# Optimization experiments

Measured on AMD Instinct MI355X. Metric: run time of the kernel, lower is better.

The kernel has to match this reference:

```python
import jax, jax.numpy as jnp
import numpy as np


def setup_inputs() -> dict:
    key = jax.random.key(0)
    ks = jax.random.split(key, 5)
    B, C, H, W = 8, 256, 64, 64
    Ck = C // 8  # 32, reduced channel dim
    return {
        "x": jax.random.normal(ks[0], (B, C, H, W), dtype=jnp.float32),
        "wf": jax.random.normal(ks[1], (Ck, C), dtype=jnp.float32) * 0.05,
        "wg": jax.random.normal(ks[2], (Ck, C), dtype=jnp.float32) * 0.05,
        "wh": jax.random.normal(ks[3], (Ck, C), dtype=jnp.float32) * 0.05,
        "wv": jax.random.normal(ks[4], (C, Ck), dtype=jnp.float32) * 0.05,
        "gamma": jnp.zeros((1,), dtype=jnp.float32),
    }


def reference(x, wf, wg, wh, wv, gamma):
    B, C, H, W = x.shape
    N = H * W
    xf = x.reshape(B, C, N)  # flatten spatial tokens
    # 1x1 convs == channel matmuls
    f = jnp.einsum('oc,bcn->bon', wf, xf)  # [B, Ck, N]
    g = jnp.einsum('oc,bcn->bon', wg, xf)  # [B, Ck, N]
    h = jnp.einsum('oc,bcn->bon', wh, xf)  # [B, Ck, N]
    # s = f^T @ g -> [B, N, N]; softmax over last axis (dim 2 in torch)
    s = jnp.einsum('bcn,bcm->bnm', f, g)
    beta = jax.nn.softmax(s, axis=2)
    # v = h @ beta  (note: beta NOT transposed, faithful to original)
    v = jnp.einsum('bcn,bnm->bcm', h, beta)  # [B, Ck, N]
    o = jnp.einsum('oc,bcm->bom', wv, v).reshape(B, C, H, W)
    return gamma * o + x
```

## Files before the change

kernel.cpp:

```cpp
#include <hip/hip_runtime.h>
#include <hip/hip_bf16.h>

#define BB 8
#define CC 256
#define CK 32
#define NN 4096

typedef short bf16x8 __attribute__((ext_vector_type(8)));
typedef float f32x4 __attribute__((ext_vector_type(4)));

#define MFMA(a, b, c) __builtin_amdgcn_mfma_f32_16x16x32_bf16((a), (b), (c), 0, 0, 0)

#define GLOAD16(gsrc, ldst) __builtin_amdgcn_global_load_lds( \
    (const __attribute__((address_space(1))) void*)(gsrc), \
    (__attribute__((address_space(3))) void*)(ldst), 16, 0, 0)

#define OBASE(b) ((size_t)(b) * 1048576)
#define OFF_F  0
#define OFF_G  65536
#define OFF_HT 131072
#define OFF_LE 196608
#define OFF_V0 200704
#define OFF_XB 524288
#define OFF_WB 786432
#define VSTRIDE 131072

#define SHIFT 24.0f

static __device__ __forceinline__ unsigned pack_trunc(float lo, float hi) {
  unsigned ulo = __builtin_bit_cast(unsigned, lo);
  unsigned uhi = __builtin_bit_cast(unsigned, hi);
  return (uhi & 0xFFFF0000u) | (ulo >> 16);
}
static __device__ __forceinline__ unsigned pack_rne(float lo, float hi) {
  unsigned ulo = __builtin_bit_cast(unsigned, lo);
  unsigned uhi = __builtin_bit_cast(unsigned, hi);
  ulo += 0x7FFFu + ((ulo >> 16) & 1u);
  uhi += 0x7FFFu + ((uhi >> 16) & 1u);
  return (uhi & 0xFFFF0000u) | (ulo >> 16);
}
static __device__ __forceinline__ unsigned short rne16(float v) {
  unsigned u = __builtin_bit_cast(unsigned, v);
  u += 0x7FFFu + ((u >> 16) & 1u);
  return (unsigned short)(u >> 16);
}

__global__ __launch_bounds__(256) void cvt_kernel(
    const float* __restrict__ x, const float* __restrict__ wf,
    const float* __restrict__ wg, const float* __restrict__ wh,
    float* __restrict__ sc)
{
  int blk = blockIdx.x;
  int tid = threadIdx.x;
  if (blk >= 2048) {
    unsigned short* wb = (unsigned short*)(sc + OFF_WB);
    const float* srcs[3] = {wf, wg, wh};
    #pragma unroll 1
    for (int w = 0; w < 3; ++w) {
      const float* src = srcs[w];
      for (int e = tid; e < 8192; e += 256) wb[w * 8192 + e] = rne16(src[e]);
    }
    return;
  }
  __shared__ float t[64][69];
  int b = blk >> 8, r = blk & 255, nt = r >> 2, ct = r & 3;
  int n0 = nt << 6, c0 = ct << 6;
  const float* xb = x + ((size_t)b * CC + c0) * NN + n0;
  int ci0 = tid >> 4, j = (tid & 15) << 2;
  #pragma unroll
  for (int p = 0; p < 4; ++p) {
    int ci = p * 16 + ci0;
    float4 v = *(const float4*)&xb[(size_t)ci * NN + j];
    t[ci][j] = v.x; t[ci][j + 1] = v.y; t[ci][j + 2] = v.z; t[ci][j + 3] = v.w;
  }
  __syncthreads();
  int ni = tid >> 2, cq = (tid & 3) << 4;
  unsigned u[8];
  #pragma unroll
  for (int e = 0; e < 8; ++e)
    u[e] = pack_rne(t[cq + 2 * e][ni], t[cq + 2 * e + 1][ni]);
  unsigned short* xbf = (unsigned short*)(sc + OBASE(b) + OFF_XB);
  unsigned* dst = (unsigned*)(xbf + (size_t)(n0 + ni) * CC + c0 + cq);
  *(uint4*)dst       = make_uint4(u[0], u[1], u[2], u[3]);
  *(uint4*)(dst + 4) = make_uint4(u[4], u[5], u[6], u[7]);
}

__global__ __launch_bounds__(256) void projmm_kernel(float* __restrict__ sc)
{
  int tid = threadIdx.x, blk = blockIdx.x;
  int b = blk >> 6, nblk = blk & 63;
  int w = tid >> 6, lane = tid & 63, q = lane >> 4, c = lane & 15;
  int nb = (nblk << 6) + (w << 4);

  const char* xB = (const char*)(sc + OBASE(b) + OFF_XB);
  const char* wB = (const char*)(sc + OFF_WB);

  const f32x4 z4 = {0.f, 0.f, 0.f, 0.f};
  f32x4 fa0 = z4, fa1 = z4, ga0 = z4, ga1 = z4, ha0 = z4, ha1 = z4;

  #pragma unroll
  for (int kc = 0; kc < 8; ++kc) {
    int ko = kc * 64 + q * 16;
    bf16x8 xa = *(const bf16x8*)(xB + (size_t)(nb + c) * 512 + ko);
    bf16x8 w0 = *(const bf16x8*)(wB + (size_t)c * 512 + ko);
    bf16x8 w1 = *(const bf16x8*)(wB + (size_t)(16 + c) * 512 + ko);
    bf16x8 w2 = *(const bf16x8*)(wB + 16384 + (size_t)c * 512 + ko);
    bf16x8 w3 = *(const bf16x8*)(wB + 16384 + (size_t)(16 + c) * 512 + ko);
    bf16x8 w4 = *(const bf16x8*)(wB + 32768 + (size_t)c * 512 + ko);
    bf16x8 w5 = *(const bf16x8*)(wB + 32768 + (size_t)(16 + c) * 512 + ko);
    fa0 = MFMA(xa, w0, fa0);  fa1 = MFMA(xa, w1, fa1);
    ga0 = MFMA(xa, w2, ga0);  ga1 = MFMA(xa, w3, ga1);
    ha0 = MFMA(w4, xa, ha0);  ha1 = MFMA(w5, xa, ha1);
  }

  unsigned short* fD = (unsigned short*)(sc + OBASE(b) + OFF_F);
  unsigned short* gD = (unsigned short*)(sc + OBASE(b) + OFF_G);
  unsigned short* hD = (unsigned short*)(sc + OBASE(b) + OFF_HT);
  #pragma unroll
  for (int r = 0; r < 4; ++r) {
    int n = nb + q * 4 + r;
    fD[(size_t)n * 32 + c]      = rne16(fa0[r]);
    fD[(size_t)n * 32 + 16 + c] = rne16(fa1[r]);
    gD[(size_t)n * 32 + c]      = rne16(ga0[r]);
    gD[(size_t)n * 32 + 16 + c] = rne16(ga1[r]);
    hD[(size_t)(q * 4 + r) * NN + nb + c]        = rne16(ha0[r]);
    hD[(size_t)(16 + q * 4 + r) * NN + nb + c]   = rne16(ha1[r]);
  }
}

__global__ __launch_bounds__(256) void passb_kernel(float* __restrict__ sc)
{
  __shared__ float Zsh[2][16][4];
  int tid = threadIdx.x, blk = blockIdx.x;
  int b = blk >> 7, nb0 = (blk & 127) << 5;
  int w = tid >> 6, lane = tid & 63, q = lane >> 4, c = lane & 15;

  const char* fb = (const char*)(sc + OBASE(b) + OFF_F);
  const char* gb = (const char*)(sc + OBASE(b) + OFF_G);

  bf16x8 fa0 = *(const bf16x8*)(fb + (size_t)(nb0 + c) * 64 + q * 16);
  bf16x8 fa1 = *(const bf16x8*)(fb + (size_t)(nb0 + 16 + c) * 64 + q * 16);
  const f32x4 z4 = {0.f, 0.f, 0.f, 0.f};
  float za[2][4] = {{0.f,0.f,0.f,0.f},{0.f,0.f,0.f,0.f}};

  int mt0 = w << 10;
  bf16x8 g0 = *(const bf16x8*)(gb + (size_t)(mt0 + 0  + c) * 64 + q * 16);
  bf16x8 g1 = *(const bf16x8*)(gb + (size_t)(mt0 + 16 + c) * 64 + q * 16);
  bf16x8 g2 = *(const bf16x8*)(gb + (size_t)(mt0 + 32 + c) * 64 + q * 16);
  bf16x8 g3 = *(const bf16x8*)(gb + (size_t)(mt0 + 48 + c) * 64 + q * 16);

  for (int mt = mt0; mt < mt0 + 1024; mt += 64) {
    int mtn = (mt + 64 < mt0 + 1024) ? mt + 64 : mt0;
    bf16x8 n0 = *(const bf16x8*)(gb + (size_t)(mtn + 0  + c) * 64 + q * 16);
    bf16x8 n1 = *(const bf16x8*)(gb + (size_t)(mtn + 16 + c) * 64 + q * 16);
    bf16x8 n2 = *(const bf16x8*)(gb + (size_t)(mtn + 32 + c) * 64 + q * 16);
    bf16x8 n3 = *(const bf16x8*)(gb + (size_t)(mtn + 48 + c) * 64 + q * 16);
    f32x4 s;
    #define BSTEP(gk) \
      s = MFMA(fa0, gk, z4); \
      za[0][0] += __expf(s[0] - SHIFT); za[0][1] += __expf(s[1] - SHIFT); \
      za[0][2] += __expf(s[2] - SHIFT); za[0][3] += __expf(s[3] - SHIFT); \
      s = MFMA(fa1, gk, z4); \
      za[1][0] += __expf(s[0] - SHIFT); za[1][1] += __expf(s[1] - SHIFT); \
      za[1][2] += __expf(s[2] - SHIFT); za[1][3] += __expf(s[3] - SHIFT);
    BSTEP(g0) BSTEP(g1) BSTEP(g2) BSTEP(g3)
    #undef BSTEP
    g0 = n0; g1 = n1; g2 = n2; g3 = n3;
  }
  #pragma unroll
  for (int d = 1; d < 16; d <<= 1) {
    #pragma unroll
    for (int i = 0; i < 2; ++i)
      #pragma unroll
      for (int r = 0; r < 4; ++r) za[i][r] += __shfl_xor(za[i][r], d);
  }
  if (c == 0) {
    #pragma unroll
    for (int i = 0; i < 2; ++i)
      #pragma unroll
      for (int r = 0; r < 4; ++r) Zsh[i][q * 4 + r][w] = za[i][r];
  }
  __syncthreads();
  if (tid < 32) {
    int ns2 = tid >> 4, row = tid & 15;
    float Z = Zsh[ns2][row][0] + Zsh[ns2][row][1]
            + Zsh[ns2][row][2] + Zsh[ns2][row][3];
    sc[OBASE(b) + OFF_LE + nb0 + ns2 * 16 + row] = SHIFT + __logf(Z);
  }
}

__global__ __launch_bounds__(256, 4) void passc_kernel(float* __restrict__ sc)
{
  __shared__ unsigned Pt[128 * 32];
  __shared__ float Lsh[1024];
  __shared__ unsigned fsh[2][1024];
  __shared__ unsigned hsh[2][1024];

  int tid = threadIdx.x, blk = blockIdx.x;
  int b = blk >> 7, rest = blk & 127;
  int ns = rest & 3, mblk = rest >> 2;
  int m0 = mblk << 7;
  int nbase = ns << 10;
  int w = tid >> 6, lane = tid & 63, q = lane >> 4, c = lane & 15;
  int hc = tid >> 3, hslot = (tid & 7) ^ (hc & 7);

  const char* fb = (const char*)(sc + OBASE(b) + OFF_F);
  const char* gb = (const char*)(sc + OBASE(b) + OFF_G);
  const char* hb = (const char*)(sc + OBASE(b) + OFF_HT);
  const float* LE = sc + OBASE(b) + OFF_LE;

  for (int i = tid; i < 1024; i += 256) Lsh[i] = LE[nbase + i];

  bf16x8 gB0 = *(const bf16x8*)(gb + (size_t)(m0 + w * 16 + c) * 64 + q * 16);
  bf16x8 gB1 = *(const bf16x8*)(gb + (size_t)(m0 + 64 + w * 16 + c) * 64 + q * 16);

  GLOAD16(fb + (size_t)nbase * 64 + tid * 16, (char*)&fsh[0][0] + tid * 16);
  GLOAD16(hb + (size_t)hc * 8192 + (size_t)nbase * 2 + hslot * 16,
          (char*)&hsh[0][0] + tid * 16);
  __syncthreads();

  const f32x4 z4 = {0.f, 0.f, 0.f, 0.f};
  f32x4 v00 = z4, v01 = z4, v10 = z4, v11 = z4;

  unsigned sw = (unsigned)(c & 7) << 4;
  char* Pt0 = (char*)Pt + (size_t)(w * 16 + c) * 128;
  char* Pt1 = (char*)Pt + (size_t)(64 + w * 16 + c) * 128;

  int buf = 0;
  for (int nt = 0; nt < 1024; nt += 64) {
    if (nt + 64 < 1024) {
      GLOAD16(fb + (size_t)(nbase + nt + 64) * 64 + tid * 16,
              (char*)&fsh[buf ^ 1][0] + tid * 16);
      GLOAD16(hb + (size_t)hc * 8192 + (size_t)(nbase + nt + 64) * 2 + hslot * 16,
              (char*)&hsh[buf ^ 1][0] + tid * 16);
    }
    const char* fS = (const char*)&fsh[buf][0];
    const char* hS = (const char*)&hsh[buf][0];

    bf16x8 f0 = *(const bf16x8*)(fS + (0 * 16 + c) * 64 + q * 16);
    bf16x8 f1 = *(const bf16x8*)(fS + (1 * 16 + c) * 64 + q * 16);
    bf16x8 f2 = *(const bf16x8*)(fS + (2 * 16 + c) * 64 + q * 16);
    bf16x8 f3 = *(const bf16x8*)(fS + (3 * 16 + c) * 64 + q * 16);
    f32x4 sA0 = MFMA(f0, gB0, z4), sB0 = MFMA(f0, gB1, z4);
    f32x4 sA1 = MFMA(f1, gB0, z4), sB1 = MFMA(f1, gB1, z4);
    f32x4 sA2 = MFMA(f2, gB0, z4), sB2 = MFMA(f2, gB1, z4);
    f32x4 sA3 = MFMA(f3, gB0, z4), sB3 = MFMA(f3, gB1, z4);

    #pragma unroll
    for (int sub = 0; sub < 4; ++sub) {
      f32x4 sA = (sub == 0) ? sA0 : (sub == 1) ? sA1 : (sub == 2) ? sA2 : sA3;
      f32x4 sB = (sub == 0) ? sB0 : (sub == 1) ? sB1 : (sub == 2) ? sB2 : sB3;
      const f32x4 Lt = *(const f32x4*)&Lsh[nt + sub * 16 + q * 4];
      uint2 pkA, pkB;
      pkA.x = pack_trunc(__expf(sA[0] - Lt[0]), __expf(sA[1] - Lt[1]));
      pkA.y = pack_trunc(__expf(sA[2] - Lt[2]), __expf(sA[3] - Lt[3]));
      pkB.x = pack_trunc(__expf(sB[0] - Lt[0]), __expf(sB[1] - Lt[1]));
      pkB.y = pack_trunc(__expf(sB[2] - Lt[2]), __expf(sB[3] - Lt[3]));
      unsigned off = ((unsigned)(sub * 32 + q * 8)) ^ sw;
      *(uint2*)(Pt0 + off) = pkA;
      *(uint2*)(Pt1 + off) = pkB;
    }

    #pragma unroll
    for (int ks = 0; ks < 2; ++ks) {
      unsigned off = ((unsigned)(ks * 64 + q * 16)) ^ sw;
      bf16x8 pb0 = *(const bf16x8*)(Pt0 + off);
      bf16x8 pb1 = *(const bf16x8*)(Pt1 + off);
      unsigned hoff = ((unsigned)(ks * 64 + q * 16)) ^ sw;
      bf16x8 h0 = *(const bf16x8*)(hS + c * 128 + hoff);
      bf16x8 h1 = *(const bf16x8*)(hS + (16 + c) * 128 + hoff);
      v00 = MFMA(h0, pb0, v00);
      v10 = MFMA(h1, pb0, v10);
      v01 = MFMA(h0, pb1, v01);
      v11 = MFMA(h1, pb1, v11);
    }
    __syncthreads();
    buf ^= 1;
  }

  float* V = sc + OBASE(b) + OFF_V0 + (size_t)ns * VSTRIDE;
  {
    int mA = m0 + w * 16 + c, mB = m0 + 64 + w * 16 + c;
    size_t bA = (size_t)(mA & 31) * 4096 + (size_t)(mA >> 5) * 32;
    size_t bB = (size_t)(mB & 31) * 4096 + (size_t)(mB >> 5) * 32;
    *(f32x4*)&V[bA + q * 4]      = v00;
    *(f32x4*)&V[bA + 16 + q * 4] = v10;
    *(f32x4*)&V[bB + q * 4]      = v01;
    *(f32x4*)&V[bB + 16 + q * 4] = v11;
  }
}

__global__ __launch_bounds__(256) void epi_kernel(
    float* out, const float* __restrict__ x,
    const float* __restrict__ wv, const float* __restrict__ gamma)
{
  int tid = threadIdx.x, blk = blockIdx.x;
  int b = blk >> 7;
  int m0 = (blk & 127) << 5;
  int w = tid >> 6, lane = tid & 63, q = lane >> 4, c = lane & 15;
  int co0 = w << 6;

  const float* V0 = out + OBASE(b) + OFF_V0;

  bf16x8 Bf[2];
  #pragma unroll
  for (int mt = 0; mt < 2; ++mt) {
    int ml = mt * 16 + c;
    size_t base = (size_t)ml * 4096 + (size_t)(m0 >> 5) * 32 + q * 8;
    float4 a0 = {0,0,0,0}, a1 = {0,0,0,0};
    #pragma unroll
    for (int i = 0; i < 4; ++i) {
      const float* Vi = V0 + (size_t)i * VSTRIDE;
      float4 p0 = *(const float4*)&Vi[base];
      float4 p1 = *(const float4*)&Vi[base + 4];
      a0.x += p0.x; a0.y += p0.y; a0.z += p0.z; a0.w += p0.w;
      a1.x += p1.x; a1.y += p1.y; a1.z += p1.z; a1.w += p1.w;
    }
    unsigned u0 = pack_rne(a0.x, a0.y);
    unsigned u1 = pack_rne(a0.z, a0.w);
    unsigned u2 = pack_rne(a1.x, a1.y);
    unsigned u3 = pack_rne(a1.z, a1.w);
    Bf[mt] = __builtin_bit_cast(bf16x8, make_uint4(u0, u1, u2, u3));
  }
  bf16x8 Af[4];
  #pragma unroll
  for (int ci = 0; ci < 4; ++ci) {
    const float* wr = wv + (size_t)(co0 + ci * 16 + c) * 32 + q * 8;
    float4 a0 = *(const float4*)wr;
    float4 a1 = *(const float4*)(wr + 4);
    unsigned u0 = pack_rne(a0.x, a0.y);
    unsigned u1 = pack_rne(a0.z, a0.w);
    unsigned u2 = pack_rne(a1.x, a1.y);
    unsigned u3 = pack_rne(a1.z, a1.w);
    Af[ci] = __builtin_bit_cast(bf16x8, make_uint4(u0, u1, u2, u3));
  }
  __syncthreads();

  const f32x4 z4 = {0.f, 0.f, 0.f, 0.f};
  const float g0 = gamma[0];
  #pragma unroll
  for (int ci = 0; ci < 4; ++ci) {
    #pragma unroll
    for (int mt = 0; mt < 2; ++mt) {
      f32x4 acc = MFMA(Af[ci], Bf[mt], z4);
      #pragma unroll
      for (int r = 0; r < 4; ++r) {
        int co = co0 + ci * 16 + q * 4 + r;
        size_t idx = ((size_t)b * CC + co) * NN + m0 + mt * 16 + c;
        out[idx] = g0 * acc[r] + x[idx];
      }
    }
  }
}

extern "C" void kernel_launch(void* const* d_in, const int* in_sizes, int n_in,
                              void* d_out, int out_size, void* d_ws, size_t ws_size,
                              hipStream_t stream) {
  const float* x     = (const float*)d_in[0];
  const float* wf    = (const float*)d_in[1];
  const float* wg    = (const float*)d_in[2];
  const float* wh    = (const float*)d_in[3];
  const float* wv    = (const float*)d_in[4];
  const float* gamma = (const float*)d_in[5];
  float* out = (float*)d_out;

  cvt_kernel   <<<2049, 256, 0, stream>>>(x, wf, wg, wh, out);
  projmm_kernel<<<512,  256, 0, stream>>>(out);
  passb_kernel <<<1024, 256, 0, stream>>>(out);
  passc_kernel <<<1024, 256, 0, stream>>>(out);
  epi_kernel   <<<1024, 256, 0, stream>>>(out, x, wv, gamma);
}
```

Before: 120.6 us.

## Fold softmax normalizer into h, use exp2 and hardware bf16 pack in passc

Pass B now computes 1/Z per query row and scales the transposed h values in place by it, so pass C no longer loads per-row log-normalizers or subtracts them before exponentiation. Exponentials switch to exp2 with a fused multiply-add against a constant shift, and packing to bf16 uses the hardware v_cvt_pk_bf16_f32 instruction. The f tile in LDS gets an XOR swizzle to cut bank conflicts, and passc's occupancy hint rises from 4 to 5. The trade-off is an extra rounding of h to bf16 after normalization, plus a fixed shift that must keep exp2 inside range.

Result: slower. 143.4 us (+19.0%).

```diff
diff --git a/kernel.cpp b/kernel.cpp
--- a/kernel.cpp
+++ b/kernel.cpp
@@ -19,19 +19,14 @@
 #define OFF_F  0
 #define OFF_G  65536
 #define OFF_HT 131072
-#define OFF_LE 196608
 #define OFF_V0 200704
 #define OFF_XB 524288
 #define OFF_WB 786432
 #define VSTRIDE 131072
 
-#define SHIFT 24.0f
-
-static __device__ __forceinline__ unsigned pack_trunc(float lo, float hi) {
-  unsigned ulo = __builtin_bit_cast(unsigned, lo);
-  unsigned uhi = __builtin_bit_cast(unsigned, hi);
-  return (uhi & 0xFFFF0000u) | (ulo >> 16);
-}
+#define L2E 1.44269504089f
+#define S2  34.6246810188f
+
 static __device__ __forceinline__ unsigned pack_rne(float lo, float hi) {
   unsigned ulo = __builtin_bit_cast(unsigned, lo);
   unsigned uhi = __builtin_bit_cast(unsigned, hi);
@@ -43,6 +38,14 @@
   unsigned u = __builtin_bit_cast(unsigned, v);
   u += 0x7FFFu + ((u >> 16) & 1u);
   return (unsigned short)(u >> 16);
+}
+static __device__ __forceinline__ unsigned pk_bf162(float lo, float hi) {
+  unsigned r;
+  asm("v_cvt_pk_bf16_f32 %0, %1, %2" : "=v"(r) : "v"(lo), "v"(hi));
+  return r;
+}
+static __device__ __forceinline__ float fexp2(float y) {
+  return __builtin_exp2f(y);
 }
 
 __global__ __launch_bounds__(256) void cvt_kernel(
@@ -131,6 +134,7 @@
 __global__ __launch_bounds__(256) void passb_kernel(float* __restrict__ sc)
 {
   __shared__ float Zsh[2][16][4];
+  __shared__ float Rsh[32];
   int tid = threadIdx.x, blk = blockIdx.x;
   int b = blk >> 7, nb0 = (blk & 127) << 5;
   int w = tid >> 6, lane = tid & 63, q = lane >> 4, c = lane & 15;
@@ -158,11 +162,11 @@
     f32x4 s;
     #define BSTEP(gk) \
       s = MFMA(fa0, gk, z4); \
-      za[0][0] += __expf(s[0] - SHIFT); za[0][1] += __expf(s[1] - SHIFT); \
-      za[0][2] += __expf(s[2] - SHIFT); za[0][3] += __expf(s[3] - SHIFT); \
+      za[0][0] += fexp2(fmaf(s[0], L2E, -S2)); za[0][1] += fexp2(fmaf(s[1], L2E, -S2)); \
+      za[0][2] += fexp2(fmaf(s[2], L2E, -S2)); za[0][3] += fexp2(fmaf(s[3], L2E, -S2)); \
       s = MFMA(fa1, gk, z4); \
-      za[1][0] += __expf(s[0] - SHIFT); za[1][1] += __expf(s[1] - SHIFT); \
-      za[1][2] += __expf(s[2] - SHIFT); za[1][3] += __expf(s[3] - SHIFT);
+      za[1][0] += fexp2(fmaf(s[0], L2E, -S2)); za[1][1] += fexp2(fmaf(s[1], L2E, -S2)); \
+      za[1][2] += fexp2(fmaf(s[2], L2E, -S2)); za[1][3] += fexp2(fmaf(s[3], L2E, -S2));
     BSTEP(g0) BSTEP(g1) BSTEP(g2) BSTEP(g3)
     #undef BSTEP
     g0 = n0; g1 = n1; g2 = n2; g3 = n3;
@@ -185,14 +189,28 @@
     int ns2 = tid >> 4, row = tid & 15;
     float Z = Zsh[ns2][row][0] + Zsh[ns2][row][1]
             + Zsh[ns2][row][2] + Zsh[ns2][row][3];
-    sc[OBASE(b) + OFF_LE + nb0 + ns2 * 16 + row] = SHIFT + __logf(Z);
-  }
-}
-
-__global__ __launch_bounds__(256, 4) void passc_kernel(float* __restrict__ sc)
+    Rsh[ns2 * 16 + row] = 1.0f / Z;
+  }
+  __syncthreads();
+  {
+    int cidx = tid >> 3, jj = (tid & 7) << 2;
+    unsigned short* hp = (unsigned short*)(sc + OBASE(b) + OFF_HT)
+                       + (size_t)cidx * NN + nb0 + jj;
+    uint2 hv = *(const uint2*)hp;
+    float h0 = __builtin_bit_cast(float, hv.x << 16)          * Rsh[jj + 0];
+    float h1 = __builtin_bit_cast(float, hv.x & 0xFFFF0000u)  * Rsh[jj + 1];
+    float h2 = __builtin_bit_cast(float, hv.y << 16)          * Rsh[jj + 2];
+    float h3 = __builtin_bit_cast(float, hv.y & 0xFFFF0000u)  * Rsh[jj + 3];
+    uint2 ov;
+    ov.x = pack_rne(h0, h1);
+    ov.y = pack_rne(h2, h3);
+    *(uint2*)hp = ov;
+  }
+}
+
+__global__ __launch_bounds__(256, 5) void passc_kernel(float* __restrict__ sc)
 {
   __shared__ unsigned Pt[128 * 32];
-  __shared__ float Lsh[1024];
   __shared__ unsigned fsh[2][1024];
   __shared__ unsigned hsh[2][1024];
 
@@ -203,18 +221,18 @@
   int nbase = ns << 10;
   int w = tid >> 6, lane = tid & 63, q = lane >> 4, c = lane & 15;
   int hc = tid >> 3, hslot = (tid & 7) ^ (hc & 7);
+  size_t fso = (size_t)(tid >> 2) * 64
+             + (size_t)(((tid & 3) ^ ((tid >> 3) & 3)) * 16);
+  int fsw = (c >> 1) & 3;
 
   const char* fb = (const char*)(sc + OBASE(b) + OFF_F);
   const char* gb = (const char*)(sc + OBASE(b) + OFF_G);
   const char* hb = (const char*)(sc + OBASE(b) + OFF_HT);
-  const float* LE = sc + OBASE(b) + OFF_LE;
-
-  for (int i = tid; i < 1024; i += 256) Lsh[i] = LE[nbase + i];
 
   bf16x8 gB0 = *(const bf16x8*)(gb + (size_t)(m0 + w * 16 + c) * 64 + q * 16);
   bf16x8 gB1 = *(const bf16x8*)(gb + (size_t)(m0 + 64 + w * 16 + c) * 64 + q * 16);
 
-  GLOAD16(fb + (size_t)nbase * 64 + tid * 16, (char*)&fsh[0][0] + tid * 16);
+  GLOAD16(fb + (size_t)nbase * 64 + fso, (char*)&fsh[0][0] + tid * 16);
   GLOAD16(hb + (size_t)hc * 8192 + (size_t)nbase * 2 + hslot * 16,
           (char*)&hsh[0][0] + tid * 16);
   __syncthreads();
@@ -229,7 +247,7 @@
   int buf = 0;
   for (int nt = 0; nt < 1024; nt += 64) {
     if (nt + 64 < 1024) {
-      GLOAD16(fb + (size_t)(nbase + nt + 64) * 64 + tid * 16,
+      GLOAD16(fb + (size_t)(nbase + nt + 64) * 64 + fso,
               (char*)&fsh[buf ^ 1][0] + tid * 16);
       GLOAD16(hb + (size_t)hc * 8192 + (size_t)(nbase + nt + 64) * 2 + hslot * 16,
               (char*)&hsh[buf ^ 1][0] + tid * 16);
@@ -237,10 +255,10 @@
     const char* fS = (const char*)&fsh[buf][0];
     const char* hS = (const char*)&hsh[buf][0];
 
-    bf16x8 f0 = *(const bf16x8*)(fS + (0 * 16 + c) * 64 + q * 16);
-    bf16x8 f1 = *(const bf16x8*)(fS + (1 * 16 + c) * 64 + q * 16);
-    bf16x8 f2 = *(const bf16x8*)(fS + (2 * 16 + c) * 64 + q * 16);
-    bf16x8 f3 = *(const bf16x8*)(fS + (3 * 16 + c) * 64 + q * 16);
+    bf16x8 f0 = *(const bf16x8*)(fS + (size_t)(0 * 16 + c) * 64 + ((q ^ fsw) * 16));
+    bf16x8 f1 = *(const bf16x8*)(fS + (size_t)(1 * 16 + c) * 64 + ((q ^ fsw) * 16));
+    bf16x8 f2 = *(const bf16x8*)(fS + (size_t)(2 * 16 + c) * 64 + ((q ^ fsw) * 16));
+    bf16x8 f3 = *(const bf16x8*)(fS + (size_t)(3 * 16 + c) * 64 + ((q ^ fsw) * 16));
     f32x4 sA0 = MFMA(f0, gB0, z4), sB0 = MFMA(f0, gB1, z4);
     f32x4 sA1 = MFMA(f1, gB0, z4), sB1 = MFMA(f1, gB1, z4);
     f32x4 sA2 = MFMA(f2, gB0, z4), sB2 = MFMA(f2, gB1, z4);
@@ -250,12 +268,11 @@
     for (int sub = 0; sub < 4; ++sub) {
       f32x4 sA = (sub == 0) ? sA0 : (sub == 1) ? sA1 : (sub == 2) ? sA2 : sA3;
       f32x4 sB = (sub == 0) ? sB0 : (sub == 1) ? sB1 : (sub == 2) ? sB2 : sB3;
-      const f32x4 Lt = *(const f32x4*)&Lsh[nt + sub * 16 + q * 4];
       uint2 pkA, pkB;
-      pkA.x = pack_trunc(__expf(sA[0] - Lt[0]), __expf(sA[1] - Lt[1]));
-      pkA.y = pack_trunc(__expf(sA[2] - Lt[2]), __expf(sA[3] - Lt[3]));
-      pkB.x = pack_trunc(__expf(sB[0] - Lt[0]), __expf(sB[1] - Lt[1]));
-      pkB.y = pack_trunc(__expf(sB[2] - Lt[2]), __expf(sB[3] - Lt[3]));
+      pkA.x = pk_bf162(fexp2(fmaf(sA[0], L2E, -S2)), fexp2(fmaf(sA[1], L2E, -S2)));
+      pkA.y = pk_bf162(fexp2(fmaf(sA[2], L2E, -S2)), fexp2(fmaf(sA[3], L2E, -S2)));
+      pkB.x = pk_bf162(fexp2(fmaf(sB[0], L2E, -S2)), fexp2(fmaf(sB[1], L2E, -S2)));
+      pkB.y = pk_bf162(fexp2(fmaf(sB[2], L2E, -S2)), fexp2(fmaf(sB[3], L2E, -S2)));
       unsigned off = ((unsigned)(sub * 32 + q * 8)) ^ sw;
       *(uint2*)(Pt0 + off) = pkA;
       *(uint2*)(Pt1 + off) = pkB;
@@ -266,9 +283,8 @@
       unsigned off = ((unsigned)(ks * 64 + q * 16)) ^ sw;
       bf16x8 pb0 = *(const bf16x8*)(Pt0 + off);
       bf16x8 pb1 = *(const bf16x8*)(Pt1 + off);
-      unsigned hoff = ((unsigned)(ks * 64 + q * 16)) ^ sw;
-      bf16x8 h0 = *(const bf16x8*)(hS + c * 128 + hoff);
-      bf16x8 h1 = *(const bf16x8*)(hS + (16 + c) * 128 + hoff);
+      bf16x8 h0 = *(const bf16x8*)(hS + c * 128 + off);
+      bf16x8 h1 = *(const bf16x8*)(hS + (16 + c) * 128 + off);
       v00 = MFMA(h0, pb0, v00);
       v10 = MFMA(h1, pb0, v10);
       v01 = MFMA(h0, pb1, v01);
```

## Fuse x-to-bf16 conversion into projection kernel via shared memory

Applied to the files above, without the earlier changes.

The x transpose and bf16 conversion now happen inside the projection kernel, which stages a 64-token by 256-channel bf16 tile in shared memory and feeds the MFMAs from it. This removes the global write and read of a bf16 copy of x, and weight conversion becomes a separate tiny 3-block kernel. In exchange each projection block loops over four channel tiles serially with two barriers each, and uses about 51KB of LDS, which lowers occupancy. A redundant offset computation in passc is also folded.

Result: faster. 108.8 us (-9.7%).

```diff
diff --git a/kernel.cpp b/kernel.cpp
--- a/kernel.cpp
+++ b/kernel.cpp
@@ -21,7 +21,6 @@
 #define OFF_HT 131072
 #define OFF_LE 196608
 #define OFF_V0 200704
-#define OFF_XB 524288
 #define OFF_WB 786432
 #define VSTRIDE 131072
 
@@ -45,63 +44,58 @@
   return (unsigned short)(u >> 16);
 }
 
-__global__ __launch_bounds__(256) void cvt_kernel(
-    const float* __restrict__ x, const float* __restrict__ wf,
-    const float* __restrict__ wg, const float* __restrict__ wh,
-    float* __restrict__ sc)
-{
-  int blk = blockIdx.x;
+__global__ __launch_bounds__(256) void wcvt_kernel(
+    const float* __restrict__ wf, const float* __restrict__ wg,
+    const float* __restrict__ wh, float* __restrict__ sc)
+{
+  int w = blockIdx.x;
   int tid = threadIdx.x;
-  if (blk >= 2048) {
-    unsigned short* wb = (unsigned short*)(sc + OFF_WB);
-    const float* srcs[3] = {wf, wg, wh};
-    #pragma unroll 1
-    for (int w = 0; w < 3; ++w) {
-      const float* src = srcs[w];
-      for (int e = tid; e < 8192; e += 256) wb[w * 8192 + e] = rne16(src[e]);
-    }
-    return;
-  }
+  const float* src = (w == 0) ? wf : ((w == 1) ? wg : wh);
+  unsigned short* wb = (unsigned short*)(sc + OFF_WB) + w * 8192;
+  for (int e = tid; e < 8192; e += 256) wb[e] = rne16(src[e]);
+}
+
+__global__ __launch_bounds__(256) void proj_kernel(
+    const float* __restrict__ x, float* __restrict__ sc)
+{
   __shared__ float t[64][69];
-  int b = blk >> 8, r = blk & 255, nt = r >> 2, ct = r & 3;
-  int n0 = nt << 6, c0 = ct << 6;
-  const float* xb = x + ((size_t)b * CC + c0) * NN + n0;
-  int ci0 = tid >> 4, j = (tid & 15) << 2;
-  #pragma unroll
-  for (int p = 0; p < 4; ++p) {
-    int ci = p * 16 + ci0;
-    float4 v = *(const float4*)&xb[(size_t)ci * NN + j];
-    t[ci][j] = v.x; t[ci][j + 1] = v.y; t[ci][j + 2] = v.z; t[ci][j + 3] = v.w;
-  }
-  __syncthreads();
-  int ni = tid >> 2, cq = (tid & 3) << 4;
-  unsigned u[8];
-  #pragma unroll
-  for (int e = 0; e < 8; ++e)
-    u[e] = pack_rne(t[cq + 2 * e][ni], t[cq + 2 * e + 1][ni]);
-  unsigned short* xbf = (unsigned short*)(sc + OBASE(b) + OFF_XB);
-  unsigned* dst = (unsigned*)(xbf + (size_t)(n0 + ni) * CC + c0 + cq);
-  *(uint4*)dst       = make_uint4(u[0], u[1], u[2], u[3]);
-  *(uint4*)(dst + 4) = make_uint4(u[4], u[5], u[6], u[7]);
-}
-
-__global__ __launch_bounds__(256) void projmm_kernel(float* __restrict__ sc)
-{
+  __shared__ unsigned short tb[64][264];
+
   int tid = threadIdx.x, blk = blockIdx.x;
-  int b = blk >> 6, nblk = blk & 63;
+  int b = blk >> 6, n0 = (blk & 63) << 6;
+
+  #pragma unroll 1
+  for (int ct = 0; ct < 4; ++ct) {
+    int c0 = ct << 6;
+    const float* xb = x + ((size_t)b * CC + c0) * NN + n0;
+    int ci0 = tid >> 4, j = (tid & 15) << 2;
+    #pragma unroll
+    for (int p = 0; p < 4; ++p) {
+      int ci = p * 16 + ci0;
+      float4 v = *(const float4*)&xb[(size_t)ci * NN + j];
+      t[ci][j] = v.x; t[ci][j + 1] = v.y; t[ci][j + 2] = v.z; t[ci][j + 3] = v.w;
+    }
+    __syncthreads();
+    int ni = tid >> 2, cq = (tid & 3) << 4;
+    #pragma unroll
+    for (int e = 0; e < 16; ++e)
+      tb[ni][c0 + cq + e] = rne16(t[cq + e][ni]);
+    __syncthreads();
+  }
+
   int w = tid >> 6, lane = tid & 63, q = lane >> 4, c = lane & 15;
-  int nb = (nblk << 6) + (w << 4);
-
-  const char* xB = (const char*)(sc + OBASE(b) + OFF_XB);
+  int nb = n0 + (w << 4);
   const char* wB = (const char*)(sc + OFF_WB);
+  const unsigned short* tbrow = &tb[(w << 4) + c][0];
 
   const f32x4 z4 = {0.f, 0.f, 0.f, 0.f};
   f32x4 fa0 = z4, fa1 = z4, ga0 = z4, ga1 = z4, ha0 = z4, ha1 = z4;
 
   #pragma unroll
   for (int kc = 0; kc < 8; ++kc) {
+    int koe = kc * 32 + q * 8;
     int ko = kc * 64 + q * 16;
-    bf16x8 xa = *(const bf16x8*)(xB + (size_t)(nb + c) * 512 + ko);
+    bf16x8 xa = *(const bf16x8*)(tbrow + koe);
     bf16x8 w0 = *(const bf16x8*)(wB + (size_t)c * 512 + ko);
     bf16x8 w1 = *(const bf16x8*)(wB + (size_t)(16 + c) * 512 + ko);
     bf16x8 w2 = *(const bf16x8*)(wB + 16384 + (size_t)c * 512 + ko);
@@ -266,9 +260,8 @@
       unsigned off = ((unsigned)(ks * 64 + q * 16)) ^ sw;
       bf16x8 pb0 = *(const bf16x8*)(Pt0 + off);
       bf16x8 pb1 = *(const bf16x8*)(Pt1 + off);
-      unsigned hoff = ((unsigned)(ks * 64 + q * 16)) ^ sw;
-      bf16x8 h0 = *(const bf16x8*)(hS + c * 128 + hoff);
-      bf16x8 h1 = *(const bf16x8*)(hS + (16 + c) * 128 + hoff);
+      bf16x8 h0 = *(const bf16x8*)(hS + c * 128 + off);
+      bf16x8 h1 = *(const bf16x8*)(hS + (16 + c) * 128 + off);
       v00 = MFMA(h0, pb0, v00);
       v10 = MFMA(h1, pb0, v10);
       v01 = MFMA(h0, pb1, v01);
@@ -364,9 +357,9 @@
   const float* gamma = (const float*)d_in[5];
   float* out = (float*)d_out;
 
-  cvt_kernel   <<<2049, 256, 0, stream>>>(x, wf, wg, wh, out);
-  projmm_kernel<<<512,  256, 0, stream>>>(out);
-  passb_kernel <<<1024, 256, 0, stream>>>(out);
-  passc_kernel <<<1024, 256, 0, stream>>>(out);
-  epi_kernel   <<<1024, 256, 0, stream>>>(out, x, wv, gamma);
-}
+  wcvt_kernel <<<3,    256, 0, stream>>>(wf, wg, wh, out);
+  proj_kernel <<<512,  256, 0, stream>>>(x, out);
+  passb_kernel<<<1024, 256, 0, stream>>>(out);
+  passc_kernel<<<1024, 256, 0, stream>>>(out);
+  epi_kernel  <<<1024, 256, 0, stream>>>(out, x, wv, gamma);
+}
```
